# Kernel optimization log

Hardware: AMD Instinct MI355X
Metric: run time of the kernel (lower is better)

## Reference

```python
import jax, jax.numpy as jnp
import numpy as np

N = 50000        # nodes
E = 800000       # edges
FEAT = 64        # cfg.feature_dim
HID = 128        # cfg.hidden_dim
G = 8            # num graphs
EPS = 1e-5       # LayerNorm eps
MIN_DEPTH, MAX_DEPTH = 0.1, 3.0


def _ln(x, g, b):
    m = jnp.mean(x, axis=-1, keepdims=True)
    v = jnp.mean((x - m) ** 2, axis=-1, keepdims=True)
    return (x - m) * jax.lax.rsqrt(v + EPS) * g + b


def setup_inputs() -> dict:
    key = jax.random.key(0)
    ks = jax.random.split(key, 32)
    f32 = jnp.float32
    inp = {}
    inp['x'] = jax.random.normal(ks[0], (N, FEAT), dtype=f32)
    inp['edge_index'] = jax.random.randint(ks[1], (2, E), 0, N)
    inp['batch'] = jnp.sort(jax.random.randint(ks[2], (N,), 0, G))
    # input_projection: Linear(FEAT,HID) + LayerNorm
    inp['in_w'] = jax.random.normal(ks[3], (FEAT, HID), dtype=f32) * (1.0 / np.sqrt(FEAT))
    inp['in_b'] = jnp.zeros((HID,), f32)
    inp['in_ln_g'] = jnp.ones((HID,), f32)
    inp['in_ln_b'] = jnp.zeros((HID,), f32)
    # epigenetics
    inp['methylation'] = jnp.zeros((HID,), f32)
    inp['histones'] = jnp.zeros((4,), f32)
    inp['log_depth'] = jnp.zeros((), f32)
    # NeuralODEFunc: 3 stacked GCNConv(HID,HID) + LayerNorms, gate MLP, residual scalar
    inp['gcn_w'] = jax.random.normal(ks[4], (3, HID, HID), dtype=f32) * (1.0 / np.sqrt(HID))
    inp['gcn_b'] = jnp.zeros((3, HID), f32)
    inp['ln_g'] = jnp.ones((3, HID), f32)
    inp['ln_b'] = jnp.zeros((3, HID), f32)
    inp['gate_w'] = jax.random.normal(ks[5], (2 * HID, HID), dtype=f32) * (1.0 / np.sqrt(2 * HID))
    inp['gate_b'] = jnp.zeros((HID,), f32)
    inp['residual_weight'] = jnp.asarray(0.1, f32)
    # output_projection: Linear(HID,HID) + LayerNorm
    inp['out_w'] = jax.random.normal(ks[6], (HID, HID), dtype=f32) * (1.0 / np.sqrt(HID))
    inp['out_b'] = jnp.zeros((HID,), f32)
    inp['out_ln_g'] = jnp.ones((HID,), f32)
    inp['out_ln_b'] = jnp.zeros((HID,), f32)
    return inp


def reference(x, edge_index, batch, in_w, in_b, in_ln_g, in_ln_b, methylation,
              histones, log_depth, gcn_w, gcn_b, ln_g, ln_b, gate_w, gate_b,
              residual_weight, out_w, out_b, out_ln_g, out_ln_b):
    n = x.shape[0]
    src, dst = edge_index[0], edge_index[1]

    # input_projection (Dropout is identity in eval)
    h = jax.nn.relu(_ln(x @ in_w + in_b, in_ln_g, in_ln_b))

    # epigenetic regulation (chromatin_accessibility goes through .item() -> constant)
    meth_sil = jnp.mean(jax.nn.sigmoid(methylation))
    hm = jax.nn.sigmoid(histones)
    act = (hm[0] + hm[2]) * 0.5
    rep = (hm[1] + hm[3]) * 0.5
    chrom = jax.lax.stop_gradient(jnp.clip(act - rep + 0.5, 0.0, 1.0))
    h = h * (chrom * (1.0 - meth_sil))

    # symmetric GCN normalization, no self loops (computed once, no grad path)
    deg = jax.ops.segment_sum(jnp.ones((E,), h.dtype), dst, num_segments=n)
    dinv = jnp.where(deg > 0, jax.lax.rsqrt(jnp.maximum(deg, 1.0)), 0.0)
    enorm = (dinv[src] * dinv[dst])[:, None]  # [E,1]

    def gcn(hh, i):
        xw = hh @ gcn_w[i]                                   # [N,H]
        agg = jax.ops.segment_sum(xw[src] * enorm, dst, num_segments=n)
        return agg + gcn_b[i]

    def ode_f(hh):
        h_orig = hh
        cur = hh
        for i in range(3):  # fixed layer count
            h_new = _ln(gcn(cur, i), ln_g[i], ln_b[i])
            if i > 0:
                gate = jax.nn.sigmoid(
                    jnp.concatenate([cur, h_new], axis=-1) @ gate_w + gate_b)
                cur = gate * h_new + (1.0 - gate) * cur
            else:
                cur = h_new
        cur = jnp.tanh(cur)
        return cur + residual_weight * h_orig

    # depth via .item() in torch -> non-differentiable constant
    depth = jax.lax.stop_gradient(
        jnp.clip(jnp.exp(log_depth), MIN_DEPTH, MAX_DEPTH))
    # single fixed RK4 step over t = linspace(0, depth, 2)
    dt = depth
    k1 = ode_f(h)
    k2 = ode_f(h + 0.5 * dt * k1)
    k3 = ode_f(h + 0.5 * dt * k2)
    k4 = ode_f(h + dt * k3)
    h_final = h + (dt / 6.0) * (k1 + 2.0 * k2 + 2.0 * k3 + k4)

    # output_projection + global_mean_pool over batch
    h_out = _ln(h_final @ out_w + out_b, out_ln_g, out_ln_b)
    cnt = jax.ops.segment_sum(jnp.ones((n,), h.dtype), batch, num_segments=G)
    pooled = jax.ops.segment_sum(h_out, batch, num_segments=G)
    return pooled / jnp.maximum(cnt, 1.0)[:, None]
```

## Files before the change

kernel.cpp:

```cpp
#include <hip/hip_runtime.h>
#include <math.h>

#define NN 50000
#define EE 800000
#define HH 128
#define FF 64
#define GG 8
#define PB 500

using short8 = __attribute__((ext_vector_type(8))) short;
using f32x4  = __attribute__((ext_vector_type(4))) float;
using f32x2  = __attribute__((ext_vector_type(2))) float;

__device__ __forceinline__ float sigm(float x){ return 1.0f/(1.0f+expf(-x)); }
__device__ __forceinline__ unsigned short f2bf(float f){
    union { float f; unsigned u; } v; v.f = f;
    unsigned r = v.u + 0x7fff + ((v.u >> 16) & 1);
    return (unsigned short)(r >> 16);
}
__device__ __forceinline__ float bf2f(unsigned short h){
    union { unsigned u; float f; } v; v.u = ((unsigned)h) << 16;
    return v.f;
}

#if __has_builtin(__builtin_amdgcn_cvt_pk_fp8_f32) && __has_builtin(__builtin_amdgcn_cvt_pk_f32_fp8)
#define FP8_HW 1
#else
#define FP8_HW 0
#endif

__device__ __forceinline__ unsigned fp8enc1_sw(float f){
    union { float fl; unsigned u; } x; x.fl = f;
    unsigned s = (x.u >> 31) << 7;
    float a = fabsf(f);
    if (!(a > 0.f)) return s;
    if (a >= 448.f) return s | 0x7E;
    if (a < 0.015625f) {
        int q = (int)(a * 512.f + 0.5f);
        if (q > 7) return s | (1u << 3);
        return s | (unsigned)q;
    }
    unsigned u = x.u + (1u << 19);
    int e32 = (int)((u >> 23) & 255) - 127;
    if (e32 < -6) { int q=(int)(a*512.f+0.5f); if(q>7)q=7; return s|(unsigned)q; }
    if (e32 > 8) return s | 0x7E;
    unsigned m = (u >> 20) & 7;
    return s | ((unsigned)(e32 + 7) << 3) | m;
}
__device__ __forceinline__ float fp8dec1_sw(unsigned v){
    unsigned s = v >> 7, e = (v >> 3) & 15, m = v & 7;
    float f;
    if (e == 0) f = (float)m * 0.001953125f;
    else { union { unsigned u; float fl; } x; x.u = ((e + 120u) << 23) | (m << 20); f = x.fl; }
    return s ? -f : f;
}
__device__ __forceinline__ unsigned char e2fp8(float a){
#if FP8_HW
    return (unsigned char)(__builtin_amdgcn_cvt_pk_fp8_f32(a, a, 0, false) & 0xFF);
#else
    return (unsigned char)fp8enc1_sw(a);
#endif
}
__device__ __forceinline__ float2 d2fp8(unsigned short u){
#if FP8_HW
    f32x2 r = __builtin_amdgcn_cvt_pk_f32_fp8((int)(unsigned)u, false);
    return make_float2(r[0], r[1]);
#else
    return make_float2(fp8dec1_sw(u & 0xFF), fp8dec1_sw((u >> 8) & 0xFF));
#endif
}

__global__ void k_setup(const float* __restrict__ meth,
                        const float* __restrict__ histones,
                        const float* __restrict__ logd,
                        float* __restrict__ scal)
{
    int l = threadIdx.x;
    float s = sigm(meth[l]) + sigm(meth[l + 64]);
#pragma unroll
    for (int o = 32; o >= 1; o >>= 1) s += __shfl_xor(s, o, 64);
    if (l == 0) {
        float msil = s * (1.0f / 128.0f);
        float h0 = sigm(histones[0]), h1 = sigm(histones[1]);
        float h2 = sigm(histones[2]), h3 = sigm(histones[3]);
        float act = (h0 + h2) * 0.5f, rep = (h1 + h3) * 0.5f;
        float chrom = fminf(fmaxf(act - rep + 0.5f, 0.0f), 1.0f);
        scal[0] = chrom * (1.0f - msil);
        float d = expf(logd[0]);
        scal[1] = fminf(fmaxf(d, 0.1f), 3.0f);
    }
}

__global__ void k_pack(const float* __restrict__ W, unsigned short* __restrict__ out, int K)
{
    int i = blockIdx.x * 256 + threadIdx.x;
    if (i >= K * 128) return;
    int k = i >> 7, n = i & 127;
    int c = k >> 5, kl = k & 31, q = kl >> 3, j = kl & 7;
    int b = n >> 4, ln = n & 15;
    int lane = q * 16 + ln;
    out[((c * 8 + b) * 64 + lane) * 8 + j] = f2bf(W[i]);
}

__global__ void k_cvtx(const float* __restrict__ x, unsigned short* __restrict__ xb)
{
    size_t i = (size_t)blockIdx.x * 256 + threadIdx.x;
    if (i >= (size_t)NN * 16) return;
    float4 v = ((const float4*)x)[i];
    ushort4 o;
    o.x = f2bf(v.x); o.y = f2bf(v.y); o.z = f2bf(v.z); o.w = f2bf(v.w);
    ((ushort4*)xb)[i] = o;
}

__global__ void k_hist(const int* __restrict__ ei, int* __restrict__ hist)
{
    int e = blockIdx.x * 256 + threadIdx.x;
    if (e < EE) atomicAdd(&hist[ei[EE + e]], 1);
}

__global__ void k_dinv(const int* __restrict__ hist, float* __restrict__ dinv)
{
    int n = blockIdx.x * 256 + threadIdx.x;
    if (n < NN) {
        int d = hist[n];
        dinv[n] = d > 0 ? rsqrtf((float)d) : 0.0f;
    }
}

__global__ void k_scan_a(const int* __restrict__ hist, int* __restrict__ aux)
{
    __shared__ int sh[256];
    int b = blockIdx.x, t = threadIdx.x;
    int base = b * 1024 + t * 4;
    int s = 0;
#pragma unroll
    for (int j = 0; j < 4; ++j) { int i = base + j; if (i < NN) s += hist[i]; }
    sh[t] = s; __syncthreads();
    for (int o = 128; o >= 1; o >>= 1) { if (t < o) sh[t] += sh[t + o]; __syncthreads(); }
    if (t == 0) aux[b] = sh[0];
}

__global__ void k_scan_b(int* __restrict__ aux, int nb)
{
    if (blockIdx.x == 0 && threadIdx.x == 0) {
        int run = 0;
        for (int i = 0; i < nb; ++i) { int v = aux[i]; aux[i] = run; run += v; }
    }
}

__global__ void k_scan_c(const int* __restrict__ hist, const int* __restrict__ aux,
                         int* __restrict__ row_ptr)
{
    __shared__ int sh[256];
    int b = blockIdx.x, t = threadIdx.x;
    int base = b * 1024 + t * 4;
    int v[4]; int s = 0;
#pragma unroll
    for (int j = 0; j < 4; ++j) { int i = base + j; v[j] = (i < NN) ? hist[i] : 0; s += v[j]; }
    sh[t] = s; __syncthreads();
    for (int o = 1; o < 256; o <<= 1) {
        int x = 0; if (t >= o) x = sh[t - o];
        __syncthreads(); sh[t] += x; __syncthreads();
    }
    int run = aux[b] + sh[t] - s;
#pragma unroll
    for (int j = 0; j < 4; ++j) { int i = base + j; if (i < NN) row_ptr[i] = run; run += v[j]; }
    if (b == 0 && t == 0) row_ptr[NN] = EE;
}

__global__ void k_scatter(const int* __restrict__ ei, const float* __restrict__ dinv,
                          int* __restrict__ cursor, uint2* __restrict__ ew)
{
    int e = blockIdx.x * 256 + threadIdx.x;
    if (e >= EE) return;
    int s = ei[e], d = ei[EE + e];
    int p = atomicAdd(&cursor[d], 1);
    ew[p] = make_uint2((unsigned)(s & 0xFFFF) | ((unsigned)(d & 63) << 16),
                       __float_as_uint(dinv[s] * dinv[d]));
}

__global__ void k_bounds(const int* __restrict__ batch, int* __restrict__ st)
{
    int g = threadIdx.x;
    if (g > GG) return;
    int lo = 0, hi = NN;
    while (lo < hi) { int mid = (lo + hi) >> 1; if (batch[mid] < g) lo = mid + 1; else hi = mid; }
    st[g] = lo;
}

template<int KC, int MODE>
__global__ __launch_bounds__(256) void k_dense_mfma(
    const unsigned short* __restrict__ A, const unsigned short* __restrict__ Wp,
    const float* __restrict__ bias, const float* __restrict__ lng,
    const float* __restrict__ lnb, const float* __restrict__ scal,
    unsigned short* __restrict__ out, unsigned char* __restrict__ out8)
{
    __shared__ unsigned short Ws[KC * 4096];
    const int t = threadIdx.x;
    {
        const float4* src = (const float4*)Wp;
        float4* dst = (float4*)Ws;
#pragma unroll
        for (int i = 0; i < KC * 2; ++i) dst[t + i * 256] = src[t + i * 256];
    }
    __syncthreads();
    const int wave = t >> 6, lane = t & 63;
    const int quad = lane >> 4, ln = lane & 15;
    const int r0 = blockIdx.x * 64 + wave * 16;
    const int K = KC * 32;
    const int arow = r0 + ln;
    const bool av = arow < NN;

    f32x4 acc[8] = {};
#pragma unroll
    for (int c = 0; c < KC; ++c) {
        short8 a = {};
        if (av) a = *(const short8*)(A + (size_t)arow * K + c * 32 + quad * 8);
#pragma unroll
        for (int b = 0; b < 8; ++b) {
            short8 bb = *(const short8*)&Ws[((c * 8 + b) * 64 + lane) * 8];
            acc[b] = __builtin_amdgcn_mfma_f32_16x16x32_bf16(a, bb, acc[b], 0, 0, 0);
        }
    }

    float b_s[8], g_s[8], e_s[8];
#pragma unroll
    for (int b = 0; b < 8; ++b) {
        int col = b * 16 + ln;
        b_s[b] = bias[col]; g_s[b] = lng[col]; e_s[b] = lnb[col];
    }
    float sc = (MODE == 1) ? scal[0] : 0.0f;
#pragma unroll
    for (int i = 0; i < 4; ++i) {
        int row = r0 + quad * 4 + i;
        float v[8]; float s = 0.f, q = 0.f;
#pragma unroll
        for (int b = 0; b < 8; ++b) { float x = acc[b][i] + b_s[b]; v[b] = x; s += x; q += x * x; }
#pragma unroll
        for (int o = 1; o < 16; o <<= 1) { s += __shfl_xor(s, o, 64); q += __shfl_xor(q, o, 64); }
        float m  = s * (1.0f / 128.0f);
        float vr = q * (1.0f / 128.0f) - m * m;
        float rs = rsqrtf(vr + 1e-5f);
        if (row < NN) {
#pragma unroll
            for (int b = 0; b < 8; ++b) {
                float o2 = (v[b] - m) * rs * g_s[b] + e_s[b];
                if (MODE == 1) o2 = fmaxf(o2, 0.f) * sc;
                out[(size_t)row * 128 + b * 16 + ln] = f2bf(o2);
                if (out8) out8[(size_t)row * 128 + b * 16 + ln] = e2fp8(o2);
            }
        }
    }
}

__global__ __launch_bounds__(256) void k_spgemm(
    const int* __restrict__ rp, const uint2* __restrict__ ew,
    const unsigned char* __restrict__ X8, const unsigned short* __restrict__ Wp,
    const float* __restrict__ bias, const float* __restrict__ lng,
    const float* __restrict__ lnb, unsigned short* __restrict__ out,
    unsigned char* __restrict__ out8)
{
    __shared__ float accf[64 * 132];
    const int t = threadIdx.x, wave = t >> 6, lane = t & 63;
    const int quad = lane >> 4, ln = lane & 15;
    const int n0 = blockIdx.x * 64;
    const int nf = n0 + wave * 16;

    {
        float* z = accf + wave * 16 * 132;
        for (int i = lane; i < 16 * 132; i += 64) z[i] = 0.f;
    }

    if (nf < NN) {
        const int nl = min(nf + 16, NN);
        const int ebeg = __builtin_amdgcn_readfirstlane(rp[nf]);
        const int eend = __builtin_amdgcn_readfirstlane(rp[nl]);
        if (ebeg < eend) {
            float2 r0a = make_float2(0.f, 0.f), r1a = make_float2(0.f, 0.f);
            int curd = (int)((ew[ebeg].x >> 16) & 63u);
            const unsigned char* Xl = X8 + lane * 2;
            uint2 rcur[8];
#pragma unroll
            for (int u = 0; u < 8; ++u) rcur[u] = ew[ebeg + u];
            for (int e = ebeg; e < eend; e += 8) {
                const int m = min(8, eend - e);
                uint2 rnxt[8];
#pragma unroll
                for (int u = 0; u < 8; ++u) rnxt[u] = ew[e + 8 + u];
                float2 g[8];
#pragma unroll
                for (int u = 0; u < 8; ++u) {
                    int src = (int)(rcur[u].x & 0xFFFFu);
                    unsigned short v = *(const unsigned short*)(Xl + (size_t)src * 128);
                    g[u] = d2fp8(v);
                }
#pragma unroll
                for (int u = 0; u < 8; ++u) {
                    if (u >= m) break;
                    int dl = (int)((rcur[u].x >> 16) & 63u);
                    float wt = __uint_as_float(rcur[u].y);
                    if (dl != curd) {
                        *(float2*)&accf[curd * 132 + lane * 2] =
                            make_float2(r0a.x + r1a.x, r0a.y + r1a.y);
                        r0a = make_float2(0.f, 0.f);
                        r1a = make_float2(0.f, 0.f);
                        curd = dl;
                    }
                    if (u & 1) {
                        r1a.x = fmaf(wt, g[u].x, r1a.x);
                        r1a.y = fmaf(wt, g[u].y, r1a.y);
                    } else {
                        r0a.x = fmaf(wt, g[u].x, r0a.x);
                        r0a.y = fmaf(wt, g[u].y, r0a.y);
                    }
                }
#pragma unroll
                for (int u = 0; u < 8; ++u) rcur[u] = rnxt[u];
            }
            *(float2*)&accf[curd * 132 + lane * 2] =
                make_float2(r0a.x + r1a.x, r0a.y + r1a.y);
        }
    }

    f32x4 acc[8] = {};
    const float* ar = accf + ((size_t)(wave * 16 + ln)) * 132;
#pragma unroll
    for (int c = 0; c < 4; ++c) {
        float4 a0 = *(const float4*)(ar + c * 32 + quad * 8);
        float4 a1 = *(const float4*)(ar + c * 32 + quad * 8 + 4);
        short8 af;
        af[0] = (short)f2bf(a0.x); af[1] = (short)f2bf(a0.y);
        af[2] = (short)f2bf(a0.z); af[3] = (short)f2bf(a0.w);
        af[4] = (short)f2bf(a1.x); af[5] = (short)f2bf(a1.y);
        af[6] = (short)f2bf(a1.z); af[7] = (short)f2bf(a1.w);
#pragma unroll
        for (int b = 0; b < 8; ++b) {
            short8 bb = *(const short8*)(Wp + ((size_t)(c * 8 + b) * 64 + lane) * 8);
            acc[b] = __builtin_amdgcn_mfma_f32_16x16x32_bf16(af, bb, acc[b], 0, 0, 0);
        }
    }

    float b_s[8], g_s[8], e_s[8];
#pragma unroll
    for (int b = 0; b < 8; ++b) {
        int col = b * 16 + ln;
        b_s[b] = bias[col]; g_s[b] = lng[col]; e_s[b] = lnb[col];
    }
#pragma unroll
    for (int i = 0; i < 4; ++i) {
        int row = n0 + wave * 16 + quad * 4 + i;
        float v[8]; float s = 0.f, q = 0.f;
#pragma unroll
        for (int b = 0; b < 8; ++b) { float x = acc[b][i] + b_s[b]; v[b] = x; s += x; q += x * x; }
#pragma unroll
        for (int o = 1; o < 16; o <<= 1) { s += __shfl_xor(s, o, 64); q += __shfl_xor(q, o, 64); }
        float m  = s * (1.0f / 128.0f);
        float vr = q * (1.0f / 128.0f) - m * m;
        float rs = rsqrtf(vr + 1e-5f);
        if (row < NN) {
#pragma unroll
            for (int b = 0; b < 8; ++b) {
                float o2 = (v[b] - m) * rs * g_s[b] + e_s[b];
                out[(size_t)row * 128 + b * 16 + ln] = f2bf(o2);
                if (out8) out8[(size_t)row * 128 + b * 16 + ln] = e2fp8(o2);
            }
        }
    }
}

__global__ __launch_bounds__(256) void k_gate_mfma(
    unsigned short* __restrict__ cur, const unsigned short* __restrict__ hnew,
    const unsigned short* __restrict__ Wp, const float* __restrict__ gb,
    unsigned char* __restrict__ cur8)
{
    __shared__ unsigned short Ws[16384];
    const int t = threadIdx.x;
    const int wave = t >> 6, lane = t & 63;
    const int quad = lane >> 4, ln = lane & 15;
    const int r0 = blockIdx.x * 64 + wave * 16;
    const int arow = r0 + ln;
    const bool av = arow < NN;

    f32x4 acc[8] = {};
#pragma unroll
    for (int s = 0; s < 2; ++s) {
        __syncthreads();
        {
            const float4* src = (const float4*)(Wp + (size_t)s * 16384);
            float4* dst = (float4*)Ws;
#pragma unroll
            for (int i = 0; i < 8; ++i) dst[t + i * 256] = src[t + i * 256];
        }
        __syncthreads();
        const unsigned short* A = s ? hnew : cur;
#pragma unroll
        for (int c = 0; c < 4; ++c) {
            short8 a = {};
            if (av) a = *(const short8*)(A + (size_t)arow * 128 + c * 32 + quad * 8);
#pragma unroll
            for (int b = 0; b < 8; ++b) {
                short8 bb = *(const short8*)&Ws[((c * 8 + b) * 64 + lane) * 8];
                acc[b] = __builtin_amdgcn_mfma_f32_16x16x32_bf16(a, bb, acc[b], 0, 0, 0);
            }
        }
    }

    float gb_s[8];
#pragma unroll
    for (int b = 0; b < 8; ++b) gb_s[b] = gb[b * 16 + ln];
#pragma unroll
    for (int i = 0; i < 4; ++i) {
        int row = r0 + quad * 4 + i;
        if (row < NN) {
#pragma unroll
            for (int b = 0; b < 8; ++b) {
                size_t idx = (size_t)row * 128 + b * 16 + ln;
                float g  = sigm(acc[b][i] + gb_s[b]);
                float cu = bf2f(cur[idx]);
                float hn = bf2f(hnew[idx]);
                float r  = g * hn + (1.f - g) * cu;
                cur[idx]  = f2bf(r);
                cur8[idx] = e2fp8(r);
            }
        }
    }
}

template<int S>
__global__ __launch_bounds__(256) void k_stage(
    const unsigned short* __restrict__ cur, const unsigned short* __restrict__ fin,
    const unsigned short* __restrict__ h0, float* __restrict__ acc,
    unsigned short* __restrict__ ybuf, const float* __restrict__ scal,
    const float* __restrict__ rwp, unsigned char* __restrict__ y8)
{
    size_t i = (size_t)blockIdx.x * 256 + threadIdx.x;
    if (i >= (size_t)NN * 32) return;
    float dt = scal[1], rw = rwp[0];
    float wk = (S == 1 || S == 4) ? dt * (1.f / 6.f) : dt * (1.f / 3.f);
    ushort4 c4 = ((const ushort4*)cur)[i];
    ushort4 f4 = ((const ushort4*)fin)[i];
    ushort4 h4 = ((const ushort4*)h0)[i];
    float tv[4];
    tv[0] = tanhf(bf2f(c4.x)) + rw * bf2f(f4.x);
    tv[1] = tanhf(bf2f(c4.y)) + rw * bf2f(f4.y);
    tv[2] = tanhf(bf2f(c4.z)) + rw * bf2f(f4.z);
    tv[3] = tanhf(bf2f(c4.w)) + rw * bf2f(f4.w);
    float4 a;
    if (S == 1) { a.x = wk*tv[0]; a.y = wk*tv[1]; a.z = wk*tv[2]; a.w = wk*tv[3]; }
    else {
        a = ((const float4*)acc)[i];
        a.x += wk*tv[0]; a.y += wk*tv[1]; a.z += wk*tv[2]; a.w += wk*tv[3];
    }
    ((float4*)acc)[i] = a;
    float h[4] = { bf2f(h4.x), bf2f(h4.y), bf2f(h4.z), bf2f(h4.w) };
    float yv[4];
    if (S == 4) {
        yv[0] = h[0] + a.x; yv[1] = h[1] + a.y; yv[2] = h[2] + a.z; yv[3] = h[3] + a.w;
    } else {
        float cn = (S == 3) ? dt : 0.5f * dt;
        yv[0] = h[0] + cn*tv[0]; yv[1] = h[1] + cn*tv[1];
        yv[2] = h[2] + cn*tv[2]; yv[3] = h[3] + cn*tv[3];
    }
    ushort4 y;
    y.x = f2bf(yv[0]); y.y = f2bf(yv[1]); y.z = f2bf(yv[2]); y.w = f2bf(yv[3]);
    ((ushort4*)ybuf)[i] = y;
    uchar4 y8v;
    y8v.x = e2fp8(yv[0]); y8v.y = e2fp8(yv[1]);
    y8v.z = e2fp8(yv[2]); y8v.w = e2fp8(yv[3]);
    ((uchar4*)y8)[i] = y8v;
}

__global__ __launch_bounds__(128) void k_pool1(
    const unsigned short* __restrict__ h, const int* __restrict__ batch,
    float* __restrict__ partial)
{
    int c = threadIdx.x, b = blockIdx.x;
    int r0 = b * (NN / PB), r1 = r0 + (NN / PB);
    float acc = 0.f; int g = batch[r0];
#pragma unroll 4
    for (int r = r0; r < r1; ++r) {
        int gg = batch[r];
        if (gg != g) { partial[(size_t)b * 1024 + g * 128 + c] = acc; acc = 0.f; g = gg; }
        acc += bf2f(h[(size_t)r * 128 + c]);
    }
    partial[(size_t)b * 1024 + g * 128 + c] = acc;
}

__global__ __launch_bounds__(256) void k_pool2(
    const float* __restrict__ partial, const int* __restrict__ st,
    float* __restrict__ out)
{
    __shared__ float sh[8][32];
    int cb = blockIdx.x & 3, g = blockIdx.x >> 2;
    int cl = threadIdx.x & 31, sl = threadIdx.x >> 5;
    int c = cb * 32 + cl;
    float s = 0.f;
    for (int b = sl; b < PB; b += 8) s += partial[(size_t)b * 1024 + g * 128 + c];
    sh[sl][cl] = s; __syncthreads();
    if (sl == 0) {
        float tt = 0.f;
#pragma unroll
        for (int i = 0; i < 8; ++i) tt += sh[i][cl];
        int cnt = st[g + 1] - st[g];
        out[g * 128 + c] = tt / (float)(cnt > 0 ? cnt : 1);
    }
}

static inline size_t al(size_t x) { return (x + 255) & ~(size_t)255; }

extern "C" void kernel_launch(void* const* d_in, const int* in_sizes, int n_in,
                              void* d_out, int out_size, void* d_ws, size_t ws_size,
                              hipStream_t stream)
{
    const float* x       = (const float*)d_in[0];
    const int*   ei      = (const int*)d_in[1];
    const int*   batch   = (const int*)d_in[2];
    const float* in_w    = (const float*)d_in[3];
    const float* in_b    = (const float*)d_in[4];
    const float* in_lng  = (const float*)d_in[5];
    const float* in_lnb  = (const float*)d_in[6];
    const float* meth    = (const float*)d_in[7];
    const float* histn   = (const float*)d_in[8];
    const float* logd    = (const float*)d_in[9];
    const float* gcn_w   = (const float*)d_in[10];
    const float* gcn_b   = (const float*)d_in[11];
    const float* ln_g    = (const float*)d_in[12];
    const float* ln_b    = (const float*)d_in[13];
    const float* gate_w  = (const float*)d_in[14];
    const float* gate_b  = (const float*)d_in[15];
    const float* rw      = (const float*)d_in[16];
    const float* out_w   = (const float*)d_in[17];
    const float* out_b   = (const float*)d_in[18];
    const float* out_lng = (const float*)d_in[19];
    const float* out_lnb = (const float*)d_in[20];
    float* out = (float*)d_out;

    char* w = (char*)d_ws;
    size_t off = 0;
    float* scal   = (float*)(w + off); off += al(16 * 4);
    int*   hist   = (int*)(w + off);   off += al((size_t)NN * 4);
    int*   rp     = (int*)(w + off);   off += al((size_t)(NN + 1) * 4);
    int*   cursor = (int*)(w + off);   off += al((size_t)(NN + 1) * 4);
    int*   aux    = (int*)(w + off);   off += al(64 * 4);
    int*   st     = (int*)(w + off);   off += al(16 * 4);
    float* dinv   = (float*)(w + off); off += al((size_t)NN * 4);
    uint2* ew     = (uint2*)(w + off); off += al((size_t)(EE + 16) * 8);
    float* partial= (float*)(w + off); off += al((size_t)PB * 1024 * 4);
    unsigned short* inwp  = (unsigned short*)(w + off); off += al(64 * 128 * 2);
    unsigned short* gcnwp = (unsigned short*)(w + off); off += al((size_t)3 * 128 * 128 * 2);
    unsigned short* gwp   = (unsigned short*)(w + off); off += al((size_t)2 * 128 * 128 * 2);
    unsigned short* owp   = (unsigned short*)(w + off); off += al(128 * 128 * 2);
    size_t B16 = al((size_t)NN * 128 * 2);
    unsigned short* xb  = (unsigned short*)(w + off); off += al((size_t)NN * 64 * 2);
    unsigned short* h0  = (unsigned short*)(w + off); off += B16;
    unsigned short* y   = (unsigned short*)(w + off); off += B16;
    unsigned short* cur = (unsigned short*)(w + off); off += B16;
    unsigned short* t2  = (unsigned short*)(w + off); off += B16;
    float* acc = (float*)(w + off); off += al((size_t)NN * 128 * 4);
    size_t B8 = al((size_t)NN * 128);
    unsigned char* h08  = (unsigned char*)(w + off); off += B8;
    unsigned char* y8   = (unsigned char*)(w + off); off += B8;
    unsigned char* cur8 = (unsigned char*)(w + off); off += B8;
    if (off > ws_size) return;

    hipMemsetAsync(hist, 0, (size_t)NN * 4, stream);
    hipMemsetAsync(partial, 0, (size_t)PB * 1024 * 4, stream);
    hipMemsetAsync(ew + EE, 0, 16 * sizeof(uint2), stream);

    k_setup<<<1, 64, 0, stream>>>(meth, histn, logd, scal);
    k_pack<<<32, 256, 0, stream>>>(in_w, inwp, 64);
    for (int i = 0; i < 3; ++i)
        k_pack<<<64, 256, 0, stream>>>(gcn_w + (size_t)i * 128 * 128,
                                       gcnwp + (size_t)i * 128 * 128, 128);
    k_pack<<<64, 256, 0, stream>>>(gate_w, gwp, 128);
    k_pack<<<64, 256, 0, stream>>>(gate_w + 128 * 128, gwp + 128 * 128, 128);
    k_pack<<<64, 256, 0, stream>>>(out_w, owp, 128);
    k_cvtx<<<3125, 256, 0, stream>>>(x, xb);

    k_hist<<<(EE + 255) / 256, 256, 0, stream>>>(ei, hist);
    k_dinv<<<(NN + 255) / 256, 256, 0, stream>>>(hist, dinv);
    k_scan_a<<<49, 256, 0, stream>>>(hist, aux);
    k_scan_b<<<1, 1, 0, stream>>>(aux, 49);
    k_scan_c<<<49, 256, 0, stream>>>(hist, aux, rp);
    hipMemcpyAsync(cursor, rp, (size_t)(NN + 1) * 4, hipMemcpyDeviceToDevice, stream);
    k_scatter<<<(EE + 255) / 256, 256, 0, stream>>>(ei, dinv, cursor, ew);
    k_bounds<<<1, 16, 0, stream>>>(batch, st);

    const int DG = (NN + 63) / 64;
    k_dense_mfma<2, 1><<<DG, 256, 0, stream>>>(xb, inwp, in_b, in_lng, in_lnb, scal, h0, h08);

    for (int s = 1; s <= 4; ++s) {
        const unsigned short* fin = (s == 1) ? h0 : y;
        const unsigned char*  fin8 = (s == 1) ? h08 : y8;
        k_spgemm<<<DG, 256, 0, stream>>>(rp, ew, fin8, gcnwp, gcn_b, ln_g, ln_b, cur, cur8);
        for (int i = 1; i <= 2; ++i) {
            k_spgemm<<<DG, 256, 0, stream>>>(rp, ew, cur8,
                                             gcnwp + (size_t)i * 128 * 128, gcn_b + i * 128,
                                             ln_g + i * 128, ln_b + i * 128, t2, (unsigned char*)0);
            k_gate_mfma<<<DG, 256, 0, stream>>>(cur, t2, gwp, gate_b, cur8);
        }
        if (s == 1)      k_stage<1><<<6250, 256, 0, stream>>>(cur, fin, h0, acc, y, scal, rw, y8);
        else if (s == 2) k_stage<2><<<6250, 256, 0, stream>>>(cur, fin, h0, acc, y, scal, rw, y8);
        else if (s == 3) k_stage<3><<<6250, 256, 0, stream>>>(cur, fin, h0, acc, y, scal, rw, y8);
        else             k_stage<4><<<6250, 256, 0, stream>>>(cur, fin, h0, acc, y, scal, rw, y8);
    }

    k_dense_mfma<4, 0><<<DG, 256, 0, stream>>>(y, owp, out_b, out_lng, out_lnb, scal, t2, (unsigned char*)0);
    k_pool1<<<PB, 128, 0, stream>>>(t2, batch, partial);
    k_pool2<<<GG * 4, 256, 0, stream>>>(partial, st, out);
}
```

Baseline: 952.7 us.

## Shrink spgemm blocks to 16 rows and double-buffer gathered features

```diff
diff --git a/kernel.cpp b/kernel.cpp
--- a/kernel.cpp
+++ b/kernel.cpp
@@ -61,6 +61,15 @@
     return (unsigned char)fp8enc1_sw(a);
 #endif
 }
+__device__ __forceinline__ unsigned pk4fp8(float a, float b, float c, float d){
+#if FP8_HW
+    unsigned p0 = (unsigned)__builtin_amdgcn_cvt_pk_fp8_f32(a, b, 0, false);
+    unsigned p1 = (unsigned)__builtin_amdgcn_cvt_pk_fp8_f32(c, d, 0, false);
+    return (p0 & 0xFFFFu) | ((p1 & 0xFFFFu) << 16);
+#else
+    return fp8enc1_sw(a) | (fp8enc1_sw(b) << 8) | (fp8enc1_sw(c) << 16) | (fp8enc1_sw(d) << 24);
+#endif
+}
 __device__ __forceinline__ float2 d2fp8(unsigned short u){
 #if FP8_HW
     f32x2 r = __builtin_amdgcn_cvt_pk_f32_fp8((int)(unsigned)u, false);
@@ -175,7 +184,7 @@
     if (e >= EE) return;
     int s = ei[e], d = ei[EE + e];
     int p = atomicAdd(&cursor[d], 1);
-    ew[p] = make_uint2((unsigned)(s & 0xFFFF) | ((unsigned)(d & 63) << 16),
+    ew[p] = make_uint2((unsigned)(s & 0xFFFF) | ((unsigned)(d & 15) << 16),
                        __float_as_uint(dinv[s] * dinv[d]));
 }
 
@@ -253,52 +262,58 @@
     }
 }
 
-__global__ __launch_bounds__(256) void k_spgemm(
+__global__ __launch_bounds__(128) void k_spgemm(
     const int* __restrict__ rp, const uint2* __restrict__ ew,
     const unsigned char* __restrict__ X8, const unsigned short* __restrict__ Wp,
     const float* __restrict__ bias, const float* __restrict__ lng,
     const float* __restrict__ lnb, unsigned short* __restrict__ out,
     unsigned char* __restrict__ out8)
 {
-    __shared__ float accf[64 * 132];
+    __shared__ float accf[16 * 132];
     const int t = threadIdx.x, wave = t >> 6, lane = t & 63;
     const int quad = lane >> 4, ln = lane & 15;
-    const int n0 = blockIdx.x * 64;
-    const int nf = n0 + wave * 16;
+    const int n0 = blockIdx.x * 16;
+    const int nf = n0 + wave * 8;
 
     {
-        float* z = accf + wave * 16 * 132;
-        for (int i = lane; i < 16 * 132; i += 64) z[i] = 0.f;
+        float* z = accf + wave * 8 * 132;
+        for (int i = lane; i < 8 * 132; i += 64) z[i] = 0.f;
     }
 
     if (nf < NN) {
-        const int nl = min(nf + 16, NN);
+        const int nl = min(nf + 8, NN);
         const int ebeg = __builtin_amdgcn_readfirstlane(rp[nf]);
         const int eend = __builtin_amdgcn_readfirstlane(rp[nl]);
         if (ebeg < eend) {
             float2 r0a = make_float2(0.f, 0.f), r1a = make_float2(0.f, 0.f);
-            int curd = (int)((ew[ebeg].x >> 16) & 63u);
+            int curd = (int)((ew[ebeg].x >> 16) & 15u);
             const unsigned char* Xl = X8 + lane * 2;
-            uint2 rcur[8];
-#pragma unroll
-            for (int u = 0; u < 8; ++u) rcur[u] = ew[ebeg + u];
+            uint2 recA[8], recB[8]; float2 gA[8];
+#pragma unroll
+            for (int u = 0; u < 8; ++u) recA[u] = ew[ebeg + u];
+#pragma unroll
+            for (int u = 0; u < 8; ++u) recB[u] = ew[ebeg + 8 + u];
+#pragma unroll
+            for (int u = 0; u < 8; ++u) {
+                int src = (int)(recA[u].x & 0xFFFFu);
+                gA[u] = d2fp8(*(const unsigned short*)(Xl + (size_t)src * 128));
+            }
             for (int e = ebeg; e < eend; e += 8) {
+                float2 gB[8];
+#pragma unroll
+                for (int u = 0; u < 8; ++u) {
+                    int src = (int)(recB[u].x & 0xFFFFu);
+                    gB[u] = d2fp8(*(const unsigned short*)(Xl + (size_t)src * 128));
+                }
+                uint2 recC[8];
+#pragma unroll
+                for (int u = 0; u < 8; ++u) recC[u] = ew[e + 16 + u];
                 const int m = min(8, eend - e);
-                uint2 rnxt[8];
-#pragma unroll
-                for (int u = 0; u < 8; ++u) rnxt[u] = ew[e + 8 + u];
-                float2 g[8];
-#pragma unroll
-                for (int u = 0; u < 8; ++u) {
-                    int src = (int)(rcur[u].x & 0xFFFFu);
-                    unsigned short v = *(const unsigned short*)(Xl + (size_t)src * 128);
-                    g[u] = d2fp8(v);
-                }
 #pragma unroll
                 for (int u = 0; u < 8; ++u) {
                     if (u >= m) break;
-                    int dl = (int)((rcur[u].x >> 16) & 63u);
-                    float wt = __uint_as_float(rcur[u].y);
+                    int dl = (int)((recA[u].x >> 16) & 15u);
+                    float wt = __uint_as_float(recA[u].y);
                     if (dl != curd) {
                         *(float2*)&accf[curd * 132 + lane * 2] =
                             make_float2(r0a.x + r1a.x, r0a.y + r1a.y);
@@ -307,23 +322,24 @@
                         curd = dl;
                     }
                     if (u & 1) {
-                        r1a.x = fmaf(wt, g[u].x, r1a.x);
-                        r1a.y = fmaf(wt, g[u].y, r1a.y);
+                        r1a.x = fmaf(wt, gA[u].x, r1a.x);
+                        r1a.y = fmaf(wt, gA[u].y, r1a.y);
                     } else {
-                        r0a.x = fmaf(wt, g[u].x, r0a.x);
-                        r0a.y = fmaf(wt, g[u].y, r0a.y);
+                        r0a.x = fmaf(wt, gA[u].x, r0a.x);
+                        r0a.y = fmaf(wt, gA[u].y, r0a.y);
                     }
                 }
 #pragma unroll
-                for (int u = 0; u < 8; ++u) rcur[u] = rnxt[u];
+                for (int u = 0; u < 8; ++u) { recA[u] = recB[u]; recB[u] = recC[u]; gA[u] = gB[u]; }
             }
             *(float2*)&accf[curd * 132 + lane * 2] =
                 make_float2(r0a.x + r1a.x, r0a.y + r1a.y);
         }
     }
+    __syncthreads();
 
     f32x4 acc[8] = {};
-    const float* ar = accf + ((size_t)(wave * 16 + ln)) * 132;
+    const float* ar = accf + (size_t)ln * 132;
 #pragma unroll
     for (int c = 0; c < 4; ++c) {
         float4 a0 = *(const float4*)(ar + c * 32 + quad * 8);
@@ -348,7 +364,7 @@
     }
 #pragma unroll
     for (int i = 0; i < 4; ++i) {
-        int row = n0 + wave * 16 + quad * 4 + i;
+        int row = n0 + quad * 4 + i;
         float v[8]; float s = 0.f, q = 0.f;
 #pragma unroll
         for (int b = 0; b < 8; ++b) { float x = acc[b][i] + b_s[b]; v[b] = x; s += x; q += x * x; }
@@ -357,7 +373,7 @@
         float m  = s * (1.0f / 128.0f);
         float vr = q * (1.0f / 128.0f) - m * m;
         float rs = rsqrtf(vr + 1e-5f);
-        if (row < NN) {
+        if (((quad >> 1) == wave) && row < NN) {
 #pragma unroll
             for (int b = 0; b < 8; ++b) {
                 float o2 = (v[b] - m) * rs * g_s[b] + e_s[b];
@@ -464,10 +480,7 @@
     ushort4 y;
     y.x = f2bf(yv[0]); y.y = f2bf(yv[1]); y.z = f2bf(yv[2]); y.w = f2bf(yv[3]);
     ((ushort4*)ybuf)[i] = y;
-    uchar4 y8v;
-    y8v.x = e2fp8(yv[0]); y8v.y = e2fp8(yv[1]);
-    y8v.z = e2fp8(yv[2]); y8v.w = e2fp8(yv[3]);
-    ((uchar4*)y8)[i] = y8v;
+    ((unsigned*)y8)[i] = pk4fp8(yv[0], yv[1], yv[2], yv[3]);
 }
 
 __global__ __launch_bounds__(128) void k_pool1(
@@ -544,7 +557,7 @@
     int*   aux    = (int*)(w + off);   off += al(64 * 4);
     int*   st     = (int*)(w + off);   off += al(16 * 4);
     float* dinv   = (float*)(w + off); off += al((size_t)NN * 4);
-    uint2* ew     = (uint2*)(w + off); off += al((size_t)(EE + 16) * 8);
+    uint2* ew     = (uint2*)(w + off); off += al((size_t)(EE + 32) * 8);
     float* partial= (float*)(w + off); off += al((size_t)PB * 1024 * 4);
     unsigned short* inwp  = (unsigned short*)(w + off); off += al(64 * 128 * 2);
     unsigned short* gcnwp = (unsigned short*)(w + off); off += al((size_t)3 * 128 * 128 * 2);
@@ -565,7 +578,7 @@
 
     hipMemsetAsync(hist, 0, (size_t)NN * 4, stream);
     hipMemsetAsync(partial, 0, (size_t)PB * 1024 * 4, stream);
-    hipMemsetAsync(ew + EE, 0, 16 * sizeof(uint2), stream);
+    hipMemsetAsync(ew + EE, 0, 32 * sizeof(uint2), stream);
 
     k_setup<<<1, 64, 0, stream>>>(meth, histn, logd, scal);
     k_pack<<<32, 256, 0, stream>>>(in_w, inwp, 64);
@@ -587,14 +600,15 @@
     k_bounds<<<1, 16, 0, stream>>>(batch, st);
 
     const int DG = (NN + 63) / 64;
+    const int SG = (NN + 15) / 16;
     k_dense_mfma<2, 1><<<DG, 256, 0, stream>>>(xb, inwp, in_b, in_lng, in_lnb, scal, h0, h08);
 
     for (int s = 1; s <= 4; ++s) {
         const unsigned short* fin = (s == 1) ? h0 : y;
         const unsigned char*  fin8 = (s == 1) ? h08 : y8;
-        k_spgemm<<<DG, 256, 0, stream>>>(rp, ew, fin8, gcnwp, gcn_b, ln_g, ln_b, cur, cur8);
+        k_spgemm<<<SG, 128, 0, stream>>>(rp, ew, fin8, gcnwp, gcn_b, ln_g, ln_b, cur, cur8);
         for (int i = 1; i <= 2; ++i) {
-            k_spgemm<<<DG, 256, 0, stream>>>(rp, ew, cur8,
+            k_spgemm<<<SG, 128, 0, stream>>>(rp, ew, cur8,
                                              gcnwp + (size_t)i * 128 * 128, gcn_b + i * 128,
                                              ln_g + i * 128, ln_b + i * 128, t2, (unsigned char*)0);
             k_gate_mfma<<<DG, 256, 0, stream>>>(cur, t2, gwp, gate_b, cur8);
```

After: 923.9 us. 3.0% less time.
